# Optimization experiments

Measured on AMD Instinct MI355X. Metric: run time of the kernel, lower is better.

The kernel has to match this reference:

```python
import jax, jax.numpy as jnp
import numpy as np

NINP, NHID, NOUT = 400, 600, 400
HS = NHID + NOUT          # h_size = nhid + nout
NLEVELS, K, AUX_FREQ = 40, 2, 20
DILATION = [1]


def setup_inputs() -> dict:
    key = jax.random.key(0)
    ks = jax.random.split(key, 6)
    B, T = 8, 256
    bound = 0.01  # matches init_weights normal_(0, 0.01)
    return {
        "X": jax.random.normal(ks[0], (B, NINP, T), jnp.float32),
        "hid": jax.random.normal(ks[1], (B, HS, 1), jnp.float32),
        "cell": jax.random.normal(ks[2], (B, HS, 1), jnp.float32),
        "w1": jax.random.normal(ks[3], (4 * HS, NINP, K), jnp.float32) * bound,
        "w2": jax.random.normal(ks[4], (4 * HS, HS, K), jnp.float32) * bound,
        "b2": jax.random.normal(ks[5], (4 * HS,), jnp.float32) * bound,
    }


def _conv1d(x, w, d):
    # x: [B, Cin, T_padded], w: [Cout, Cin, K] -> [B, Cout, T]
    return jax.lax.conv_general_dilated(
        x, w, window_strides=(1,), padding='VALID', rhs_dilation=(d,),
        dimension_numbers=('NCH', 'OIH', 'NCH'))


def _forward(X, hid, cell, w1, w2, b2):
    B, _, T = X.shape
    ht = jnp.zeros((B, HS, T), X.dtype)
    ct = jnp.zeros((B, HS, T), X.dtype)

    # Input-side convolution is weight-tied and X never changes across levels,
    # so (like the torch dict cache) compute it once per distinct dilation.
    conv1 = {}
    for d in set(DILATION):
        pad = (K - 1) * d
        xp = jnp.pad(X, ((0, 0), (0, 0), (pad, 0)))
        conv1[d] = _conv1d(xp, w1, d)

    aux = []
    for i in range(NLEVELS):
        d = DILATION[i % len(DILATION)]
        pad = (K - 1) * d
        # causal left-pad of the hidden stream, filled with the initial hid
        z1 = jnp.concatenate([jnp.broadcast_to(hid, (B, HS, pad)), ht], axis=2)
        out = conv1[d] + _conv1d(z1, w2, d) + b2[None, :, None]  # [B, 4*HS, T]
        # shifted cell state, first d steps filled with the initial cell
        ct_1 = jnp.concatenate(
            [jnp.broadcast_to(cell, (B, HS, d)), ct[:, :, :-d]], axis=2)
        it = jax.nn.sigmoid(out[:, :HS])
        ot = jax.nn.sigmoid(out[:, HS:2 * HS])
        gt = jnp.tanh(out[:, 2 * HS:3 * HS])
        ft = jax.nn.sigmoid(out[:, 3 * HS:])
        ct = ft * ct_1 + it * gt
        ht = ot * jnp.tanh(ct)
        if i % AUX_FREQ == AUX_FREQ - 1:
            aux.append(ht[:, -NOUT:])  # [B, nout, T]

    out_main = jnp.transpose(ht[:, -NOUT:], (0, 2, 1))            # [B, T, nout]
    hc = (ht[:, :, -1:], ct[:, :, -1:])                            # ([B,HS,1], [B,HS,1])
    aux_outs = jnp.transpose(jnp.stack(aux, axis=0), (1, 0, 3, 2))  # [B, n_aux, T, nout]
    return out_main, hc, aux_outs


def reference(X, hid, cell, w1, w2, b2):
    return _forward(X, hid, cell, w1, w2, b2)
```

## Files before the change

### kernel.cpp

```cpp
#include <hip/hip_runtime.h>
#include <hip/hip_bf16.h>
#include <math.h>

typedef __bf16 bf16;
typedef __bf16 bf16x8 __attribute__((ext_vector_type(8)));
typedef __bf16 bf16x4 __attribute__((ext_vector_type(4)));
typedef float f32x4 __attribute__((ext_vector_type(4)));

#define NINP 400
#define HS   1000
#define HP   1024
#define B_   8
#define T_   256
#define NT   2048
#define K2   2048
#define K1   1024
#define M_   4096

#define HT_OFF   819200
#define CT_OFF   827200
#define AUX_OFF  835200

typedef __attribute__((address_space(1))) const void gvoid;
typedef __attribute__((address_space(3))) void lvoid;

__device__ __forceinline__ void async_copy16(void* lds, const void* g) {
  __builtin_amdgcn_global_load_lds((gvoid*)g, (lvoid*)lds, 16, 0, 0);
}

__device__ __forceinline__ float sigm(float x) { return 1.0f / (1.0f + expf(-x)); }


__global__ void repack_w1(const float* __restrict__ w1, bf16* __restrict__ W1p) {
  int idx = blockIdx.x * 256 + threadIdx.x;
  if (idx >= M_ * K1) return;
  int gr = idx >> 10, k = idx & 1023;
  int g = gr >> 10, hp = gr & (HP - 1);
  float v = 0.0f;
  if (hp < HS) {
    int c = g * HS + hp;
    if (k < 512) { if (k < NINP) v = w1[(size_t)c * (NINP * 2) + k * 2 + 0]; }
    else { int j = k - 512; if (j < NINP) v = w1[(size_t)c * (NINP * 2) + j * 2 + 1]; }
  }
  W1p[idx] = (bf16)v;
}

__global__ void repack_w2(const float* __restrict__ w2, bf16* __restrict__ W2p) {
  int idx = blockIdx.x * 256 + threadIdx.x;
  if (idx >= M_ * K2) return;
  int gr = idx >> 11, k = idx & 2047;
  int g = gr >> 10, hp = gr & (HP - 1);
  float v = 0.0f;
  if (hp < HS) {
    int c = g * HS + hp;
    if (k < HP) { if (k < HS) v = w2[(size_t)c * (HS * 2) + k * 2 + 0]; }
    else { int j = k - HP; if (j < HS) v = w2[(size_t)c * (HS * 2) + j * 2 + 1]; }
  }
  W2p[idx] = (bf16)v;
}

__global__ void build_xt(const float* __restrict__ X, bf16* __restrict__ XT) {
  int idx = blockIdx.x * 256 + threadIdx.x;
  if (idx >= NT * K1) return;
  int n = idx >> 10, k = idx & 1023;
  int b = n >> 8, t = n & (T_ - 1);
  float v = 0.0f;
  if (k < 512) { if (k < NINP && t > 0) v = X[((size_t)b * NINP + k) * T_ + t - 1]; }
  else { int j = k - 512; if (j < NINP) v = X[((size_t)b * NINP + j) * T_ + t]; }
  XT[idx] = (bf16)v;
}

__global__ void build_hc(const float* __restrict__ hid, const float* __restrict__ cell,
                         bf16* __restrict__ hidp, float* __restrict__ cellp) {
  int idx = blockIdx.x * 256 + threadIdx.x;
  if (idx >= B_ * HP) return;
  int b = idx >> 10, k = idx & (HP - 1);
  hidp[idx]  = (k < HS) ? (bf16)hid[b * HS + k] : (bf16)0.0f;
  cellp[idx] = (k < HS) ? cell[b * HS + k] : 0.0f;
}


template <bool GATED>
__global__ __launch_bounds__(256, 2) void gemm_step(
    const bf16* __restrict__ A,
    const bf16* __restrict__ Bsrc,
    const bf16* __restrict__ hidp,
    const bf16* __restrict__ CbIn,
    bf16* __restrict__ CbOut,
    const float* __restrict__ b2,
    const bf16* __restrict__ ctprev,
    const float* __restrict__ cellp,
    bf16* __restrict__ ctnew,
    bf16* __restrict__ Hnew,
    int K) {
  __shared__ bf16 As[128][64];
  __shared__ bf16 Bs[128][64];
  __shared__ bf16 Hsh[128][32];

  const int tid = threadIdx.x;
  const int w = tid >> 6;
  const int lane = tid & 63;
  const int c8 = lane & 7;
  const int dr = lane >> 3;
  const int quad = lane >> 4;
  const int col = lane & 15;
  const int swo = ((c8 - dr) & 7) * 8;

  int n0, bm;
  if (GATED) {
    const int L = blockIdx.y * gridDim.x + blockIdx.x;
    bm = (L & 7) * 4 + (L >> 7);
    n0 = ((L >> 3) & 15) * 128;
  } else {
    n0 = blockIdx.x * 128;
    bm = blockIdx.y;
  }

  f32x4 acc[8][2];
#pragma unroll
  for (int i = 0; i < 8; ++i)
#pragma unroll
    for (int j = 0; j < 2; ++j) acc[i][j] = (f32x4){0.f, 0.f, 0.f, 0.f};

  for (int k0 = 0; k0 < K; k0 += 64) {
    __syncthreads();
#pragma unroll
    for (int inst = 0; inst < 4; ++inst) {
      const int r = inst * 32 + w * 8 + dr;
      int grow;
      if (GATED) grow = (r >> 5) * HP + bm * 32 + (r & 31);
      else       grow = bm * 128 + r;
      async_copy16(&As[inst * 32 + w * 8][0], A + (size_t)grow * K + k0 + swo);

      const int n = n0 + r;
      const bf16* bp;
      if (GATED) {
        const int kk = (k0 & (HP - 1)) + swo;
        if (k0 < HP) {
          const int t = n & (T_ - 1);
          bp = (t == 0) ? (hidp + (size_t)(n >> 8) * HP + kk)
                        : (Bsrc + (size_t)(n - 1) * HP + kk);
        } else {
          bp = Bsrc + (size_t)n * HP + kk;
        }
      } else {
        bp = Bsrc + (size_t)n * K1 + k0 + swo;
      }
      async_copy16(&Bs[inst * 32 + w * 8][0], bp);
    }
    __syncthreads();
#pragma unroll
    for (int kc = 0; kc < 64; kc += 32) {
      bf16x8 av[8], bv[2];
#pragma unroll
      for (int mt = 0; mt < 8; ++mt) {
        const int rA = col + 16 * mt;
        av[mt] = *(const bf16x8*)&As[rA][(((kc >> 3) + quad + rA) & 7) * 8];
      }
#pragma unroll
      for (int nt = 0; nt < 2; ++nt) {
        const int rB = w * 32 + nt * 16 + col;
        bv[nt] = *(const bf16x8*)&Bs[rB][(((kc >> 3) + quad + rB) & 7) * 8];
      }
#pragma unroll
      for (int mt = 0; mt < 8; ++mt)
#pragma unroll
        for (int nt = 0; nt < 2; ++nt)
          acc[mt][nt] = __builtin_amdgcn_mfma_f32_16x16x32_bf16(av[mt], bv[nt], acc[mt][nt], 0, 0, 0);
    }
  }

  if (!GATED) {
    bf16 (*Csh)[16] = (bf16(*)[16])&As[0][0];
    const int g = bm >> 3;
#pragma unroll
    for (int mt = 0; mt < 8; ++mt) {
      __syncthreads();
#pragma unroll
      for (int nt = 0; nt < 2; ++nt) {
        const int nl = w * 32 + nt * 16 + col;
#pragma unroll
        for (int reg = 0; reg < 4; ++reg) {
          const int hp = (bm & 7) * 128 + mt * 16 + quad * 4 + reg;
          const float bias = (hp < HS) ? b2[g * HS + hp] : 0.0f;
          Csh[nl][quad * 4 + reg] = (bf16)(acc[mt][nt][reg] + bias);
        }
      }
      __syncthreads();
      const int colbase = ((bm & 7) * 8 + mt) * 64 + g * 16;
      const int row = tid >> 1, half = tid & 1;
      *(bf16x8*)&CbOut[(size_t)(n0 + row) * 4096 + colbase + half * 8] =
          *(const bf16x8*)&Csh[row][half * 8];
    }
  } else {
    const int h0 = bm * 32;
#pragma unroll
    for (int u = 0; u < 2; ++u) {
#pragma unroll
      for (int nt = 0; nt < 2; ++nt) {
        const int nl = w * 32 + nt * 16 + col;
        const int n = n0 + nl;
        const int b = n >> 8;
        const int t = n & (T_ - 1);
        const size_t cbase = (size_t)n * 4096 + (size_t)(bm * 2 + u) * 64 + quad * 4;
        bf16x4 cb0 = *(const bf16x4*)&CbIn[cbase + 0 * 16];
        bf16x4 cb1 = *(const bf16x4*)&CbIn[cbase + 1 * 16];
        bf16x4 cb2 = *(const bf16x4*)&CbIn[cbase + 2 * 16];
        bf16x4 cb3 = *(const bf16x4*)&CbIn[cbase + 3 * 16];
#pragma unroll
        for (int reg = 0; reg < 4; ++reg) {
          const int hh = u * 16 + quad * 4 + reg;
          const int h = h0 + hh;
          const float ci = acc[0 + u][nt][reg] + (float)cb0[reg];
          const float co = acc[2 + u][nt][reg] + (float)cb1[reg];
          const float cg = acc[4 + u][nt][reg] + (float)cb2[reg];
          const float cf = acc[6 + u][nt][reg] + (float)cb3[reg];
          const float ctold = (t == 0) ? cellp[b * HP + h]
                                       : (float)ctprev[(size_t)h * NT + (n - 1)];
          const float cn = sigm(cf) * ctold + sigm(ci) * tanhf(cg);
          ctnew[(size_t)h * NT + n] = (bf16)cn;
          Hsh[nl][hh] = (bf16)(sigm(co) * tanhf(cn));
        }
      }
    }
    __syncthreads();
#pragma unroll
    for (int it2 = 0; it2 < 4; ++it2) {
      const int idx = it2 * 256 + tid;
      const int row = idx >> 3;
      const int c4 = idx & 7;
      *(bf16x4*)&Hnew[(size_t)(n0 + row) * HP + h0 + c4 * 4] =
          *(const bf16x4*)&Hsh[row][c4 * 4];
    }
  }
}


__global__ void aux_kernel(const bf16* __restrict__ H, float* __restrict__ out, int s) {
  int idx = blockIdx.x * 256 + threadIdx.x;
  if (idx >= NT * 100) return;
  int n = idx / 100;
  int o = (idx % 100) * 4;
  int b = n >> 8, t = n & (T_ - 1);
  bf16x4 v = *(const bf16x4*)&H[(size_t)n * HP + 600 + o];
  f32x4 f = {(float)v[0], (float)v[1], (float)v[2], (float)v[3]};
  *(f32x4*)&out[AUX_OFF + ((size_t)((b * 2 + s) * T_ + t)) * 400 + o] = f;
}

__global__ void final_kernel(const bf16* __restrict__ H, const bf16* __restrict__ ct,
                             float* __restrict__ out) {
  int idx = blockIdx.x * 256 + threadIdx.x;
  if (idx < NT * 100) {
    int n = idx / 100;
    int o = (idx % 100) * 4;
    int b = n >> 8, t = n & (T_ - 1);
    bf16x4 v = *(const bf16x4*)&H[(size_t)n * HP + 600 + o];
    f32x4 f = {(float)v[0], (float)v[1], (float)v[2], (float)v[3]};
    *(f32x4*)&out[(size_t)n * 400 + o] = f;
    *(f32x4*)&out[AUX_OFF + ((size_t)((b * 2 + 1) * T_ + t)) * 400 + o] = f;
  } else {
    int j = idx - NT * 100;
    if (j < 8000) {
      int b = j / 1000, h = j % 1000;
      out[HT_OFF + j] = (float)H[(size_t)(b * T_ + 255) * HP + h];
    } else if (j < 16000) {
      int jj = j - 8000;
      int b = jj / 1000, h = jj % 1000;
      out[CT_OFF + jj] = (float)ct[(size_t)h * NT + b * T_ + 255];
    }
  }
}


extern "C" void kernel_launch(void* const* d_in, const int* in_sizes, int n_in,
                              void* d_out, int out_size, void* d_ws, size_t ws_size,
                              hipStream_t stream) {
  const float* X    = (const float*)d_in[0];
  const float* hid  = (const float*)d_in[1];
  const float* cell = (const float*)d_in[2];
  const float* w1   = (const float*)d_in[3];
  const float* w2   = (const float*)d_in[4];
  const float* b2   = (const float*)d_in[5];
  float* out = (float*)d_out;

  char* ws = (char*)d_ws;
  size_t off = 0;
  auto alloc = [&](size_t bytes) {
    void* p = ws + off;
    off += (bytes + 255) & ~(size_t)255;
    return p;
  };
  bf16* W2p    = (bf16*)alloc((size_t)M_ * K2 * 2);
  bf16* CbP    = (bf16*)alloc((size_t)NT * M_ * 2);
  bf16* Hb0    = (bf16*)alloc((size_t)NT * HP * 2);
  bf16* ctb0   = (bf16*)alloc((size_t)HP * NT * 2);
  bf16* hidp   = (bf16*)alloc((size_t)B_ * HP * 2);
  float* cellp = (float*)alloc((size_t)B_ * HP * 4);
  char* R = (char*)alloc((size_t)12 * 1024 * 1024);
  bf16* W1p  = (bf16*)R;
  bf16* XT   = (bf16*)(R + (size_t)8 * 1024 * 1024);
  bf16* ctb1 = (bf16*)R;
  bf16* Hb1  = (bf16*)(R + (size_t)4 * 1024 * 1024);

  bf16* Hb[2]  = {Hb0, Hb1};
  bf16* ctb[2] = {ctb0, ctb1};

  hipMemsetAsync(Hb[0], 0, (size_t)NT * HP * 2, stream);
  hipMemsetAsync(ctb[0], 0, (size_t)HP * NT * 2, stream);

  repack_w1<<<(M_ * K1) / 256, 256, 0, stream>>>(w1, W1p);
  repack_w2<<<(M_ * K2) / 256, 256, 0, stream>>>(w2, W2p);
  build_xt<<<(NT * K1) / 256, 256, 0, stream>>>(X, XT);
  build_hc<<<(B_ * HP) / 256, 256, 0, stream>>>(hid, cell, hidp, cellp);

  dim3 grid(NT / 128, 32);
  gemm_step<false><<<grid, 256, 0, stream>>>(W1p, XT, nullptr, nullptr, CbP, b2,
                                             nullptr, nullptr, nullptr, nullptr, K1);
  for (int i = 0; i < 40; ++i) {
    int p = i & 1;
    gemm_step<true><<<grid, 256, 0, stream>>>(W2p, Hb[p], hidp, CbP, nullptr, nullptr,
                                              ctb[p], cellp, ctb[p ^ 1], Hb[p ^ 1], K2);
    if (i == 19) aux_kernel<<<800, 256, 0, stream>>>(Hb[p ^ 1], out, 0);
  }
  final_kernel<<<(NT * 100 + 16000 + 255) / 256, 256, 0, stream>>>(Hb[0], ctb[0], out);
}
```

Before: 2.111 ms.

## Switch GEMM to 32x32 MFMA with 2x2 warp tiling and register-staged double buffering

Repacks weights so the four gate rows for each group of 8 hidden units sit together, which lets each 32x32x16 MFMA accumulator hold all four gates for one output. The wave layout becomes a 2x2 grid of 64x64 subtiles, and the async global-to-LDS copies are replaced by register-staged loads into double-buffered LDS. This lets global loads for the next K slice overlap with compute, with one barrier per iteration. The cost is twice the LDS, more registers for the staged loads, and a rewritten epilogue and CbP layout.

```diff
diff --git a/kernel.cpp b/kernel.cpp
--- a/kernel.cpp
+++ b/kernel.cpp
@@ -6,6 +6,9 @@
 typedef __bf16 bf16x8 __attribute__((ext_vector_type(8)));
 typedef __bf16 bf16x4 __attribute__((ext_vector_type(4)));
 typedef float f32x4 __attribute__((ext_vector_type(4)));
+typedef float f32x16 __attribute__((ext_vector_type(16)));
+typedef unsigned int u32;
+typedef u32 u32x4 __attribute__((ext_vector_type(4)));
 
 #define NINP 400
 #define HS   1000
@@ -21,42 +24,35 @@
 #define CT_OFF   827200
 #define AUX_OFF  835200
 
-typedef __attribute__((address_space(1))) const void gvoid;
-typedef __attribute__((address_space(3))) void lvoid;
-
-__device__ __forceinline__ void async_copy16(void* lds, const void* g) {
-  __builtin_amdgcn_global_load_lds((gvoid*)g, (lvoid*)lds, 16, 0, 0);
-}
-
 __device__ __forceinline__ float sigm(float x) { return 1.0f / (1.0f + expf(-x)); }
 
 
-__global__ void repack_w1(const float* __restrict__ w1, bf16* __restrict__ W1p) {
+__global__ void repack_w1(const float* __restrict__ w1, bf16* __restrict__ W1q) {
   int idx = blockIdx.x * 256 + threadIdx.x;
   if (idx >= M_ * K1) return;
-  int gr = idx >> 10, k = idx & 1023;
-  int g = gr >> 10, hp = gr & (HP - 1);
+  int m = idx >> 10, k = idx & 1023;
+  int g = (m >> 3) & 3, h = (m >> 5) * 8 + (m & 7);
   float v = 0.0f;
-  if (hp < HS) {
-    int c = g * HS + hp;
+  if (h < HS) {
+    int c = g * HS + h;
     if (k < 512) { if (k < NINP) v = w1[(size_t)c * (NINP * 2) + k * 2 + 0]; }
     else { int j = k - 512; if (j < NINP) v = w1[(size_t)c * (NINP * 2) + j * 2 + 1]; }
   }
-  W1p[idx] = (bf16)v;
-}
-
-__global__ void repack_w2(const float* __restrict__ w2, bf16* __restrict__ W2p) {
+  W1q[idx] = (bf16)v;
+}
+
+__global__ void repack_w2(const float* __restrict__ w2, bf16* __restrict__ W2q) {
   int idx = blockIdx.x * 256 + threadIdx.x;
   if (idx >= M_ * K2) return;
-  int gr = idx >> 11, k = idx & 2047;
-  int g = gr >> 10, hp = gr & (HP - 1);
+  int m = idx >> 11, k = idx & 2047;
+  int g = (m >> 3) & 3, h = (m >> 5) * 8 + (m & 7);
   float v = 0.0f;
-  if (hp < HS) {
-    int c = g * HS + hp;
+  if (h < HS) {
+    int c = g * HS + h;
     if (k < HP) { if (k < HS) v = w2[(size_t)c * (HS * 2) + k * 2 + 0]; }
     else { int j = k - HP; if (j < HS) v = w2[(size_t)c * (HS * 2) + j * 2 + 1]; }
   }
-  W2p[idx] = (bf16)v;
+  W2q[idx] = (bf16)v;
 }
 
 __global__ void build_xt(const float* __restrict__ X, bf16* __restrict__ XT) {
@@ -93,18 +89,18 @@
     bf16* __restrict__ ctnew,
     bf16* __restrict__ Hnew,
     int K) {
-  __shared__ bf16 As[128][64];
-  __shared__ bf16 Bs[128][64];
-  __shared__ bf16 Hsh[128][32];
+  __shared__ bf16 As[2][128][64];
+  __shared__ bf16 Bs[2][128][64];
 
   const int tid = threadIdx.x;
+  const int lane = tid & 63;
   const int w = tid >> 6;
-  const int lane = tid & 63;
-  const int c8 = lane & 7;
-  const int dr = lane >> 3;
-  const int quad = lane >> 4;
-  const int col = lane & 15;
-  const int swo = ((c8 - dr) & 7) * 8;
+  const int mh = w >> 1, nh = w & 1;
+  const int c8 = tid & 7;
+  const int sr = tid >> 3;
+  const int row32 = lane & 31;
+  const int q2 = lane >> 5;
+  const int physw = ((c8 + sr) & 7) * 8;
 
   int n0, bm;
   if (GATED) {
@@ -116,121 +112,154 @@
     bm = blockIdx.y;
   }
 
-  f32x4 acc[8][2];
-#pragma unroll
-  for (int i = 0; i < 8; ++i)
-#pragma unroll
-    for (int j = 0; j < 2; ++j) acc[i][j] = (f32x4){0.f, 0.f, 0.f, 0.f};
-
-  for (int k0 = 0; k0 < K; k0 += 64) {
+  const int NIT = K >> 6;
+  const bf16* Abase = A + (size_t)(bm * 128 + sr) * K + c8 * 8;
+
+  auto loadA = [&](int site, int k0) -> u32x4 {
+    return *(const u32x4*)(Abase + (size_t)site * 32 * K + k0);
+  };
+  auto loadB = [&](int site, int k0) -> u32x4 {
+    const int n = n0 + site * 32 + sr;
+    const bf16* bp;
+    if (GATED) {
+      if (k0 < HP) {
+        const int t = n & (T_ - 1);
+        bp = (t == 0) ? (hidp + (size_t)(n >> 8) * HP + k0)
+                      : (Bsrc + (size_t)(n - 1) * HP + k0);
+      } else {
+        bp = Bsrc + (size_t)n * HP + (k0 - HP);
+      }
+    } else {
+      bp = Bsrc + (size_t)n * K + k0;
+    }
+    return *(const u32x4*)(bp + c8 * 8);
+  };
+
+  f32x16 acc[2][2];
+#pragma unroll
+  for (int i = 0; i < 2; ++i)
+#pragma unroll
+    for (int j = 0; j < 2; ++j)
+#pragma unroll
+      for (int e = 0; e < 16; ++e) acc[i][j][e] = 0.0f;
+
+  u32x4 ra[4], rb[4];
+#pragma unroll
+  for (int s = 0; s < 4; ++s) { ra[s] = loadA(s, 0); rb[s] = loadB(s, 0); }
+#pragma unroll
+  for (int s = 0; s < 4; ++s) {
+    *(u32x4*)&As[0][s * 32 + sr][physw] = ra[s];
+    *(u32x4*)&Bs[0][s * 32 + sr][physw] = rb[s];
+  }
+
+  for (int it = 0; it < NIT; ++it) {
+    const int p = it & 1;
+    if (it + 1 < NIT) {
+      const int k0 = (it + 1) << 6;
+#pragma unroll
+      for (int s = 0; s < 4; ++s) { ra[s] = loadA(s, k0); rb[s] = loadB(s, k0); }
+    }
     __syncthreads();
 #pragma unroll
-    for (int inst = 0; inst < 4; ++inst) {
-      const int r = inst * 32 + w * 8 + dr;
-      int grow;
-      if (GATED) grow = (r >> 5) * HP + bm * 32 + (r & 31);
-      else       grow = bm * 128 + r;
-      async_copy16(&As[inst * 32 + w * 8][0], A + (size_t)grow * K + k0 + swo);
-
-      const int n = n0 + r;
-      const bf16* bp;
-      if (GATED) {
-        const int kk = (k0 & (HP - 1)) + swo;
-        if (k0 < HP) {
-          const int t = n & (T_ - 1);
-          bp = (t == 0) ? (hidp + (size_t)(n >> 8) * HP + kk)
-                        : (Bsrc + (size_t)(n - 1) * HP + kk);
-        } else {
-          bp = Bsrc + (size_t)n * HP + kk;
+    for (int kc = 0; kc < 4; ++kc) {
+      const int l = kc * 2 + q2;
+      bf16x8 av[2], bv[2];
+#pragma unroll
+      for (int mt = 0; mt < 2; ++mt) {
+        const int r = mh * 64 + mt * 32 + row32;
+        av[mt] = *(const bf16x8*)&As[p][r][((l + r) & 7) * 8];
+      }
+#pragma unroll
+      for (int nt = 0; nt < 2; ++nt) {
+        const int r = nh * 64 + nt * 32 + row32;
+        bv[nt] = *(const bf16x8*)&Bs[p][r][((l + r) & 7) * 8];
+      }
+#pragma unroll
+      for (int mt = 0; mt < 2; ++mt)
+#pragma unroll
+        for (int nt = 0; nt < 2; ++nt)
+          acc[mt][nt] = __builtin_amdgcn_mfma_f32_32x32x16_bf16(av[mt], bv[nt], acc[mt][nt], 0, 0, 0);
+    }
+    if (it + 1 < NIT) {
+      const int q = p ^ 1;
+#pragma unroll
+      for (int s = 0; s < 4; ++s) {
+        *(u32x4*)&As[q][s * 32 + sr][physw] = ra[s];
+        *(u32x4*)&Bs[q][s * 32 + sr][physw] = rb[s];
+      }
+    }
+  }
+
+  if (!GATED) {
+    __syncthreads();
+    bf16 (*Csh)[128] = (bf16(*)[128])&As[0][0][0];
+#pragma unroll
+    for (int mt = 0; mt < 2; ++mt) {
+      const int tt = mh * 2 + mt;
+#pragma unroll
+      for (int nt = 0; nt < 2; ++nt) {
+        const int nloc = nh * 64 + nt * 32 + row32;
+#pragma unroll
+        for (int g = 0; g < 4; ++g) {
+          bf16x4 v;
+#pragma unroll
+          for (int j = 0; j < 4; ++j) {
+            const int h = bm * 32 + tt * 8 + 4 * q2 + j;
+            const float bias = (h < HS) ? b2[g * HS + h] : 0.0f;
+            v[j] = (bf16)(acc[mt][nt][g * 4 + j] + bias);
+          }
+          *(bf16x4*)&Csh[nloc][tt * 32 + g * 8 + 4 * q2] = v;
         }
-      } else {
-        bp = Bsrc + (size_t)n * K1 + k0 + swo;
-      }
-      async_copy16(&Bs[inst * 32 + w * 8][0], bp);
+      }
     }
     __syncthreads();
 #pragma unroll
-    for (int kc = 0; kc < 64; kc += 32) {
-      bf16x8 av[8], bv[2];
-#pragma unroll
-      for (int mt = 0; mt < 8; ++mt) {
-        const int rA = col + 16 * mt;
-        av[mt] = *(const bf16x8*)&As[rA][(((kc >> 3) + quad + rA) & 7) * 8];
-      }
+    for (int i2 = 0; i2 < 8; ++i2) {
+      const int idx = i2 * 256 + tid;
+      const int rrow = idx >> 4, off = idx & 15;
+      *(u32x4*)&CbOut[(size_t)(n0 + rrow) * 4096 + bm * 128 + off * 8] =
+          *(const u32x4*)&Csh[rrow][off * 8];
+    }
+  } else {
+    bf16 (*Hsh)[32] = (bf16(*)[32])&As[0][0][0];
+#pragma unroll
+    for (int mt = 0; mt < 2; ++mt) {
+      const int tt = mh * 2 + mt;
 #pragma unroll
       for (int nt = 0; nt < 2; ++nt) {
-        const int rB = w * 32 + nt * 16 + col;
-        bv[nt] = *(const bf16x8*)&Bs[rB][(((kc >> 3) + quad + rB) & 7) * 8];
-      }
-#pragma unroll
-      for (int mt = 0; mt < 8; ++mt)
-#pragma unroll
-        for (int nt = 0; nt < 2; ++nt)
-          acc[mt][nt] = __builtin_amdgcn_mfma_f32_16x16x32_bf16(av[mt], bv[nt], acc[mt][nt], 0, 0, 0);
-    }
-  }
-
-  if (!GATED) {
-    bf16 (*Csh)[16] = (bf16(*)[16])&As[0][0];
-    const int g = bm >> 3;
-#pragma unroll
-    for (int mt = 0; mt < 8; ++mt) {
-      __syncthreads();
-#pragma unroll
-      for (int nt = 0; nt < 2; ++nt) {
-        const int nl = w * 32 + nt * 16 + col;
-#pragma unroll
-        for (int reg = 0; reg < 4; ++reg) {
-          const int hp = (bm & 7) * 128 + mt * 16 + quad * 4 + reg;
-          const float bias = (hp < HS) ? b2[g * HS + hp] : 0.0f;
-          Csh[nl][quad * 4 + reg] = (bf16)(acc[mt][nt][reg] + bias);
-        }
-      }
-      __syncthreads();
-      const int colbase = ((bm & 7) * 8 + mt) * 64 + g * 16;
-      const int row = tid >> 1, half = tid & 1;
-      *(bf16x8*)&CbOut[(size_t)(n0 + row) * 4096 + colbase + half * 8] =
-          *(const bf16x8*)&Csh[row][half * 8];
-    }
-  } else {
-    const int h0 = bm * 32;
-#pragma unroll
-    for (int u = 0; u < 2; ++u) {
-#pragma unroll
-      for (int nt = 0; nt < 2; ++nt) {
-        const int nl = w * 32 + nt * 16 + col;
-        const int n = n0 + nl;
+        const int nloc = nh * 64 + nt * 32 + row32;
+        const int n = n0 + nloc;
         const int b = n >> 8;
         const int t = n & (T_ - 1);
-        const size_t cbase = (size_t)n * 4096 + (size_t)(bm * 2 + u) * 64 + quad * 4;
-        bf16x4 cb0 = *(const bf16x4*)&CbIn[cbase + 0 * 16];
-        bf16x4 cb1 = *(const bf16x4*)&CbIn[cbase + 1 * 16];
-        bf16x4 cb2 = *(const bf16x4*)&CbIn[cbase + 2 * 16];
-        bf16x4 cb3 = *(const bf16x4*)&CbIn[cbase + 3 * 16];
-#pragma unroll
-        for (int reg = 0; reg < 4; ++reg) {
-          const int hh = u * 16 + quad * 4 + reg;
-          const int h = h0 + hh;
-          const float ci = acc[0 + u][nt][reg] + (float)cb0[reg];
-          const float co = acc[2 + u][nt][reg] + (float)cb1[reg];
-          const float cg = acc[4 + u][nt][reg] + (float)cb2[reg];
-          const float cf = acc[6 + u][nt][reg] + (float)cb3[reg];
+        const size_t cb = (size_t)n * 4096 + (size_t)(bm * 4 + tt) * 32 + 4 * q2;
+        bf16x4 c0 = *(const bf16x4*)&CbIn[cb + 0];
+        bf16x4 c1 = *(const bf16x4*)&CbIn[cb + 8];
+        bf16x4 c2 = *(const bf16x4*)&CbIn[cb + 16];
+        bf16x4 c3 = *(const bf16x4*)&CbIn[cb + 24];
+        bf16x4 hv;
+#pragma unroll
+        for (int j = 0; j < 4; ++j) {
+          const int h = bm * 32 + tt * 8 + 4 * q2 + j;
+          const float ci = acc[mt][nt][0 + j]  + (float)c0[j];
+          const float co = acc[mt][nt][4 + j]  + (float)c1[j];
+          const float cg = acc[mt][nt][8 + j]  + (float)c2[j];
+          const float cf = acc[mt][nt][12 + j] + (float)c3[j];
           const float ctold = (t == 0) ? cellp[b * HP + h]
                                        : (float)ctprev[(size_t)h * NT + (n - 1)];
           const float cn = sigm(cf) * ctold + sigm(ci) * tanhf(cg);
           ctnew[(size_t)h * NT + n] = (bf16)cn;
-          Hsh[nl][hh] = (bf16)(sigm(co) * tanhf(cn));
+          hv[j] = (bf16)(sigm(co) * tanhf(cn));
         }
+        *(bf16x4*)&Hsh[nloc][tt * 8 + 4 * q2] = hv;
       }
     }
     __syncthreads();
 #pragma unroll
-    for (int it2 = 0; it2 < 4; ++it2) {
-      const int idx = it2 * 256 + tid;
-      const int row = idx >> 3;
-      const int c4 = idx & 7;
-      *(bf16x4*)&Hnew[(size_t)(n0 + row) * HP + h0 + c4 * 4] =
-          *(const bf16x4*)&Hsh[row][c4 * 4];
+    for (int i2 = 0; i2 < 2; ++i2) {
+      const int idx = i2 * 256 + tid;
+      const int rrow = idx >> 2, off = idx & 3;
+      *(u32x4*)&Hnew[(size_t)(n0 + rrow) * HP + bm * 32 + off * 8] =
+          *(const u32x4*)&Hsh[rrow][off * 8];
     }
   }
 }
@@ -290,14 +319,14 @@
     off += (bytes + 255) & ~(size_t)255;
     return p;
   };
-  bf16* W2p    = (bf16*)alloc((size_t)M_ * K2 * 2);
+  bf16* W2q    = (bf16*)alloc((size_t)M_ * K2 * 2);
   bf16* CbP    = (bf16*)alloc((size_t)NT * M_ * 2);
   bf16* Hb0    = (bf16*)alloc((size_t)NT * HP * 2);
   bf16* ctb0   = (bf16*)alloc((size_t)HP * NT * 2);
   bf16* hidp   = (bf16*)alloc((size_t)B_ * HP * 2);
   float* cellp = (float*)alloc((size_t)B_ * HP * 4);
   char* R = (char*)alloc((size_t)12 * 1024 * 1024);
-  bf16* W1p  = (bf16*)R;
+  bf16* W1q  = (bf16*)R;
   bf16* XT   = (bf16*)(R + (size_t)8 * 1024 * 1024);
   bf16* ctb1 = (bf16*)R;
   bf16* Hb1  = (bf16*)(R + (size_t)4 * 1024 * 1024);
@@ -308,17 +337,17 @@
   hipMemsetAsync(Hb[0], 0, (size_t)NT * HP * 2, stream);
   hipMemsetAsync(ctb[0], 0, (size_t)HP * NT * 2, stream);
 
-  repack_w1<<<(M_ * K1) / 256, 256, 0, stream>>>(w1, W1p);
-  repack_w2<<<(M_ * K2) / 256, 256, 0, stream>>>(w2, W2p);
+  repack_w1<<<(M_ * K1) / 256, 256, 0, stream>>>(w1, W1q);
+  repack_w2<<<(M_ * K2) / 256, 256, 0, stream>>>(w2, W2q);
   build_xt<<<(NT * K1) / 256, 256, 0, stream>>>(X, XT);
   build_hc<<<(B_ * HP) / 256, 256, 0, stream>>>(hid, cell, hidp, cellp);
 
-  dim3 grid(NT / 128, 32);
-  gemm_step<false><<<grid, 256, 0, stream>>>(W1p, XT, nullptr, nullptr, CbP, b2,
+  dim3 grid(NT / 128, M_ / 128);
+  gemm_step<false><<<grid, 256, 0, stream>>>(W1q, XT, nullptr, nullptr, CbP, b2,
                                              nullptr, nullptr, nullptr, nullptr, K1);
   for (int i = 0; i < 40; ++i) {
     int p = i & 1;
-    gemm_step<true><<<grid, 256, 0, stream>>>(W2p, Hb[p], hidp, CbP, nullptr, nullptr,
+    gemm_step<true><<<grid, 256, 0, stream>>>(W2q, Hb[p], hidp, CbP, nullptr, nullptr,
                                               ctb[p], cellp, ctb[p ^ 1], Hb[p ^ 1], K2);
     if (i == 19) aux_kernel<<<800, 256, 0, stream>>>(Hb[p ^ 1], out, 0);
   }
```

New measurement: 2.140 ms. About the same (+1.4%).
